# Kernel optimization log

Hardware: AMD Instinct MI355X
Metric: run time of the kernel (lower is better)

Reference implementation:

```python
import jax, jax.numpy as jnp
import numpy as np

SEQ, BATCH = 512, 256
INPUT_WIDTH, STATE_WIDTH = 64, 960
STREAM = INPUT_WIDTH + STATE_WIDTH  # 1024
OUTPUT_WIDTH = 128
P = 0.97  # identity_proportion


def _smooth_l1(pred, target):
    # torch.nn.SmoothL1Loss (beta=1, mean reduction)
    d = jnp.abs(pred - target)
    return jnp.mean(jnp.where(d < 1.0, 0.5 * d * d, d - 0.5))


def setup_inputs() -> dict:
    key = jax.random.key(0)
    k_in, k_st, k_w1, k_w2 = jax.random.split(key, 4)
    bound = float(np.sqrt(6.0 / (STREAM + STREAM)))  # xavier_uniform, gain=1
    return {
        "input": jax.random.normal(k_in, (SEQ, BATCH, INPUT_WIDTH), dtype=jnp.float32),
        "init_state": jax.random.normal(k_st, (BATCH, STREAM), dtype=jnp.float32),
        "aff_w": jnp.ones((STREAM,), dtype=jnp.float32),
        "aff_b": jnp.zeros((STREAM,), dtype=jnp.float32),
        "fc1_w": jax.random.uniform(k_w1, (STREAM, STREAM), minval=-bound, maxval=bound, dtype=jnp.float32),
        "fc1_b": jnp.zeros((STREAM,), dtype=jnp.float32),
        "fc2_w": jax.random.uniform(k_w2, (STREAM, STREAM), minval=-bound, maxval=bound, dtype=jnp.float32),
        "fc2_b": jnp.zeros((STREAM,), dtype=jnp.float32),
    }


def reference(input, init_state, aff_w, aff_b, fc1_w, fc1_b, fc2_w, fc2_b):
    iw = input.shape[-1]

    def res(s):
        # BatchNorm-style regularizer (torch.var -> unbiased, ddof=1)
        reg = _smooth_l1(s.mean(0), 0.0) + _smooth_l1(jnp.var(s, axis=0, ddof=1), 1.0)
        h = jnp.abs(s @ fc1_w.T + fc1_b)          # [B, STREAM]
        out = P * s + (1.0 - P) * (h @ fc2_w.T + fc2_b)
        return out, reg

    # step 0: overwrite + affine + res
    s = jnp.concatenate([input[0], init_state[:, iw:]], axis=-1)
    s = aff_w * s + aff_b
    s, reg0 = res(s)

    def body(s, elem):
        s = jnp.concatenate([elem, s[:, iw:]], axis=-1)  # Overwrite
        s, reg = res(s)
        return s, reg

    s, regs = jax.lax.scan(body, s, input[1:])
    out = s[:, -OUTPUT_WIDTH:]
    reg = jnp.concatenate([reg0[None], regs]).mean()
    return out, reg
```

## Files before the change

kernel.cpp:

```cpp
#include <hip/hip_runtime.h>
#include <stdint.h>
#include <stddef.h>

#define SEQ 512
#define BATCH 256
#define IW 64
#define STREAM 1024
#define OW 128

#define NGROUP 8
#define NSLICE 32
#define CW 32
#define RPG 32
#define NT 256

typedef __attribute__((ext_vector_type(4)))  float  f32x4;
typedef __attribute__((ext_vector_type(16))) float  f32x16;
typedef __attribute__((ext_vector_type(8)))  __bf16 bf16x8;
typedef __attribute__((ext_vector_type(8)))  short  short8;

__device__ __forceinline__ unsigned short f2bf(float x) {
  union { float f; uint32_t u; } v; v.f = x;
  return (unsigned short)((v.u + 0x7FFFu + ((v.u >> 16) & 1u)) >> 16);
}
__device__ __forceinline__ uint64_t pack4bf(f32x4 v) {
  return (uint64_t)f2bf(v[0]) | ((uint64_t)f2bf(v[1]) << 16)
       | ((uint64_t)f2bf(v[2]) << 32) | ((uint64_t)f2bf(v[3]) << 48);
}
__device__ __forceinline__ f32x4 ld_mall(const void* p) {
  f32x4 r;
  asm volatile("global_load_dwordx4 %0, %1, off sc0 sc1" : "=v"(r) : "v"(p) : "memory");
  return r;
}
__device__ __forceinline__ void st_mall(void* p, uint64_t v) {
  asm volatile("global_store_dwordx2 %0, %1, off sc0 sc1" :: "v"(p), "v"(v) : "memory");
}
#define WAIT_VM(N) do { asm volatile("s_waitcnt vmcnt(" #N ")" ::: "memory"); \
                        __builtin_amdgcn_sched_barrier(0); } while (0)

__device__ __forceinline__ int xoff(int rr, int k) {
  int c = k >> 3;
  return ((c >> 1) << 10) + ((c & 1) << 9) + (rr << 4) + ((k & 4) << 1);
}

#define WS_FLAGS   0
#define WS_SUMS    4096
#define WS_SUMS2   (4096 + 2097152)
#define WS_REGT    (4096 + 4194304)
#define WS_SBUF    (4096 + 4194304 + 4096)
#define WS_HBUF    (WS_SBUF + NGROUP*RPG*STREAM*2)
#define ZERO_BYTES (4096 + 4194304)

__global__ __launch_bounds__(NT, 1) void rnn_main(
    const float* __restrict__ input, const float* __restrict__ init_state,
    const float* __restrict__ aff_w, const float* __restrict__ aff_b,
    const float* __restrict__ fc1_w, const float* __restrict__ fc1_b,
    const float* __restrict__ fc2_w, const float* __restrict__ fc2_b,
    float* __restrict__ d_out, char* __restrict__ ws)
{
  __shared__ __align__(16) short W1s[NSLICE * STREAM];
  __shared__ __align__(16) short W2s[NSLICE * STREAM];
  __shared__ __align__(16) float partial[4 * RPG * CW];
  __shared__ __align__(16) float b1s[CW], b2s[CW];

  const int tid = threadIdx.x;
  const int g = blockIdx.x & 7;
  const int j = blockIdx.x >> 3;

  uint32_t* sflag = (uint32_t*)(ws + WS_FLAGS) + g * 32;
  uint32_t* hflag = (uint32_t*)(ws + WS_FLAGS + 1024) + g * 32;
  float* sumS  = (float*)(ws + WS_SUMS);
  float* sumS2 = (float*)(ws + WS_SUMS2);
  char* sbuf_c = ws + WS_SBUF + (size_t)g * (RPG * STREAM * 2);
  char* hbuf_c = ws + WS_HBUF + (size_t)g * (RPG * STREAM * 2);

  for (int idx = tid; idx < NSLICE * (STREAM / 8); idx += NT) {
    int n = idx >> 7;
    int kc = idx & 127;
    const float* p1 = fc1_w + (size_t)(j * CW + n) * STREAM + (kc << 3);
    const float* p2 = fc2_w + (size_t)(j * CW + n) * STREAM + (kc << 3);
    f32x4 a0 = *(const f32x4*)p1, a1 = *(const f32x4*)(p1 + 4);
    f32x4 c0 = *(const f32x4*)p2, c1 = *(const f32x4*)(p2 + 4);
    short8 w1v, w2v;
#pragma unroll
    for (int i = 0; i < 4; ++i) {
      w1v[i] = (short)f2bf(a0[i]); w1v[4 + i] = (short)f2bf(a1[i]);
      w2v[i] = (short)f2bf(c0[i]); w2v[4 + i] = (short)f2bf(c1[i]);
    }
    int boff = (n << 11) + ((kc << 4) ^ ((n & 7) << 4));
    *(short8*)((char*)W1s + boff) = w1v;
    *(short8*)((char*)W2s + boff) = w2v;
  }
  if (tid < CW) {
    b1s[tid] = fc1_b[j * CW + tid];
    b2s[tid] = fc2_b[j * CW + tid];
  }

  const int rr_ = tid >> 3;
  const int c4  = (tid & 7) << 2;
  const int gc  = j * CW + c4;
  f32x4 master = {0.f, 0.f, 0.f, 0.f};

  {
    f32x4 v;
    if (j >= 2) v = *(const f32x4*)(init_state + (size_t)(g * RPG + rr_) * STREAM + gc);
    else        v = *(const f32x4*)(input + (size_t)(g * RPG + rr_) * IW + gc);
    f32x4 w  = *(const f32x4*)(aff_w + gc);
    f32x4 bb = *(const f32x4*)(aff_b + gc);
    v = w * v + bb;
    if (j >= 2) master = v;
    st_mall(sbuf_c + xoff(rr_, gc), pack4bf(v));
    *(f32x4*)(partial + (rr_ << 5) + c4) = v;
  }
  WAIT_VM(0);
  __syncthreads();
  if (tid == 0)
    __hip_atomic_fetch_add(sflag, 1u, __ATOMIC_RELAXED, __HIP_MEMORY_SCOPE_AGENT);
  if (tid < CW) {
    float s1 = 0.f, s2 = 0.f;
#pragma unroll 4
    for (int r = 0; r < RPG; ++r) { float v = partial[(r << 5) + tid]; s1 += v; s2 += v * v; }
    atomicAdd(sumS  + j * CW + tid, s1);
    atomicAdd(sumS2 + j * CW + tid, s2);
  }

  const int ln  = tid & 63;
  const int wv  = tid >> 6;
  const int ar  = ln & 31;
  const int kof = (ln >> 5) << 3;
  const int klo = wv << 8;
  const int swzB = (ar & 7) << 4;
  const char* W1c = (const char*)W1s + (ar << 11);
  const char* W2c = (const char*)W2s + (ar << 11);
  const char* pa_s = sbuf_c + (wv << 14) + (ln << 4);
  const char* pa_h = hbuf_c + (wv << 14) + (ln << 4);

  for (int t = 0; t < SEQ; ++t) {
    if (tid == 0) {
      uint32_t tgt = 32u * (t + 1);
      while (__hip_atomic_load(sflag, __ATOMIC_RELAXED, __HIP_MEMORY_SCOPE_AGENT) < tgt)
        __builtin_amdgcn_s_sleep(1);
    }
    __syncthreads();

    {
      f32x4 a[16];
#pragma unroll
      for (int it = 0; it < 16; ++it) a[it] = ld_mall(pa_s + (it << 10));
      bf16x8 bf[16];
#pragma unroll
      for (int it = 0; it < 16; ++it)
        bf[it] = *(const bf16x8*)(W1c + (((klo + (it << 4) + kof) << 1) ^ swzB));
      f32x16 acc0 = {}, acc1 = {};
      WAIT_VM(8);
#pragma unroll
      for (int it = 0; it < 8; it += 2) {
        acc0 = __builtin_amdgcn_mfma_f32_32x32x16_bf16(__builtin_bit_cast(bf16x8, a[it]),     bf[it],     acc0, 0, 0, 0);
        acc1 = __builtin_amdgcn_mfma_f32_32x32x16_bf16(__builtin_bit_cast(bf16x8, a[it + 1]), bf[it + 1], acc1, 0, 0, 0);
      }
      WAIT_VM(0);
#pragma unroll
      for (int it = 8; it < 16; it += 2) {
        acc0 = __builtin_amdgcn_mfma_f32_32x32x16_bf16(__builtin_bit_cast(bf16x8, a[it]),     bf[it],     acc0, 0, 0, 0);
        acc1 = __builtin_amdgcn_mfma_f32_32x32x16_bf16(__builtin_bit_cast(bf16x8, a[it + 1]), bf[it + 1], acc1, 0, 0, 0);
      }
      acc0 += acc1;
      float* pw = partial + (wv << 10);
#pragma unroll
      for (int i = 0; i < 16; ++i) {
        int r = (i & 3) + ((i >> 2) << 3) + ((ln >> 5) << 2);
        pw[(r << 5) + (ln & 31)] = acc0[i];
      }
    }
    __syncthreads();
    {
      f32x4 sum = *(const f32x4*)(partial + (rr_ << 5) + c4);
      sum += *(const f32x4*)(partial + 1024 + (rr_ << 5) + c4);
      sum += *(const f32x4*)(partial + 2048 + (rr_ << 5) + c4);
      sum += *(const f32x4*)(partial + 3072 + (rr_ << 5) + c4);
      f32x4 vb = *(const f32x4*)(b1s + c4);
      f32x4 hv;
#pragma unroll
      for (int i = 0; i < 4; ++i) hv[i] = fabsf(sum[i] + vb[i]);
      st_mall(hbuf_c + xoff(rr_, gc), pack4bf(hv));
    }
    WAIT_VM(0);
    __syncthreads();
    if (tid == 0)
      __hip_atomic_fetch_add(hflag, 1u, __ATOMIC_RELAXED, __HIP_MEMORY_SCOPE_AGENT);

    if (tid == 0) {
      uint32_t tgt = 32u * (t + 1);
      while (__hip_atomic_load(hflag, __ATOMIC_RELAXED, __HIP_MEMORY_SCOPE_AGENT) < tgt)
        __builtin_amdgcn_s_sleep(1);
    }
    __syncthreads();

    f32x4 nxt = {0.f, 0.f, 0.f, 0.f};
    if (j >= 2) {
      f32x4 a[16];
#pragma unroll
      for (int it = 0; it < 16; ++it) a[it] = ld_mall(pa_h + (it << 10));
      bf16x8 bf[16];
#pragma unroll
      for (int it = 0; it < 16; ++it)
        bf[it] = *(const bf16x8*)(W2c + (((klo + (it << 4) + kof) << 1) ^ swzB));
      f32x16 acc0 = {}, acc1 = {};
      WAIT_VM(8);
#pragma unroll
      for (int it = 0; it < 8; it += 2) {
        acc0 = __builtin_amdgcn_mfma_f32_32x32x16_bf16(__builtin_bit_cast(bf16x8, a[it]),     bf[it],     acc0, 0, 0, 0);
        acc1 = __builtin_amdgcn_mfma_f32_32x32x16_bf16(__builtin_bit_cast(bf16x8, a[it + 1]), bf[it + 1], acc1, 0, 0, 0);
      }
      WAIT_VM(0);
#pragma unroll
      for (int it = 8; it < 16; it += 2) {
        acc0 = __builtin_amdgcn_mfma_f32_32x32x16_bf16(__builtin_bit_cast(bf16x8, a[it]),     bf[it],     acc0, 0, 0, 0);
        acc1 = __builtin_amdgcn_mfma_f32_32x32x16_bf16(__builtin_bit_cast(bf16x8, a[it + 1]), bf[it + 1], acc1, 0, 0, 0);
      }
      acc0 += acc1;
      float* pw = partial + (wv << 10);
#pragma unroll
      for (int i = 0; i < 16; ++i) {
        int r = (i & 3) + ((i >> 2) << 3) + ((ln >> 5) << 2);
        pw[(r << 5) + (ln & 31)] = acc0[i];
      }
      __syncthreads();
      f32x4 sum = *(const f32x4*)(partial + (rr_ << 5) + c4);
      sum += *(const f32x4*)(partial + 1024 + (rr_ << 5) + c4);
      sum += *(const f32x4*)(partial + 2048 + (rr_ << 5) + c4);
      sum += *(const f32x4*)(partial + 3072 + (rr_ << 5) + c4);
      f32x4 vb = *(const f32x4*)(b2s + c4);
#pragma unroll
      for (int i = 0; i < 4; ++i)
        master[i] = 0.97f * master[i] + 0.03f * (sum[i] + vb[i]);
      if (t < SEQ - 1)
        st_mall(sbuf_c + xoff(rr_, gc), pack4bf(master));
    } else {
      if (t < SEQ - 1) {
        nxt = *(const f32x4*)(input + ((size_t)(t + 1) * BATCH + g * RPG + rr_) * IW + gc);
        st_mall(sbuf_c + xoff(rr_, gc), pack4bf(nxt));
      }
    }

    __syncthreads();
    if (t < SEQ - 1)
      *(f32x4*)(partial + (rr_ << 5) + c4) = (j >= 2) ? master : nxt;
    WAIT_VM(0);
    __syncthreads();
    if (tid == 0)
      __hip_atomic_fetch_add(sflag, 1u, __ATOMIC_RELAXED, __HIP_MEMORY_SCOPE_AGENT);
    if (t < SEQ - 1 && tid < CW) {
      float s1 = 0.f, s2 = 0.f;
#pragma unroll 4
      for (int r = 0; r < RPG; ++r) { float v = partial[(r << 5) + tid]; s1 += v; s2 += v * v; }
      atomicAdd(sumS  + (size_t)(t + 1) * STREAM + j * CW + tid, s1);
      atomicAdd(sumS2 + (size_t)(t + 1) * STREAM + j * CW + tid, s2);
    }
  }

  if (j >= 28) {
    float* dst = d_out + (size_t)(g * RPG + rr_) * OW + (j - 28) * CW + c4;
    *(f32x4*)dst = master;
  }
}

__global__ void reg_reduce1(const float* __restrict__ sumS, const float* __restrict__ sumS2,
                            float* __restrict__ regt) {
  int t = blockIdx.x;
  float acc = 0.f;
  for (int c = threadIdx.x; c < STREAM; c += 256) {
    float s1 = sumS[t * STREAM + c];
    float s2 = sumS2[t * STREAM + c];
    float m = s1 * (1.0f / 256.0f);
    float var = (s2 - 256.0f * m * m) * (1.0f / 255.0f);
    float d1 = fabsf(m);
    acc += (d1 < 1.f) ? 0.5f * d1 * d1 : d1 - 0.5f;
    float d2 = fabsf(var - 1.f);
    acc += (d2 < 1.f) ? 0.5f * d2 * d2 : d2 - 0.5f;
  }
#pragma unroll
  for (int off = 32; off > 0; off >>= 1) acc += __shfl_down(acc, off, 64);
  __shared__ float red[4];
  if ((threadIdx.x & 63) == 0) red[threadIdx.x >> 6] = acc;
  __syncthreads();
  if (threadIdx.x == 0)
    regt[t] = (red[0] + red[1] + red[2] + red[3]) * (1.0f / 1024.0f);
}

__global__ void reg_reduce2(const float* __restrict__ regt, float* __restrict__ out_reg) {
  float acc = regt[threadIdx.x] + regt[threadIdx.x + 256];
#pragma unroll
  for (int off = 32; off > 0; off >>= 1) acc += __shfl_down(acc, off, 64);
  __shared__ float red[4];
  if ((threadIdx.x & 63) == 0) red[threadIdx.x >> 6] = acc;
  __syncthreads();
  if (threadIdx.x == 0)
    out_reg[0] = (red[0] + red[1] + red[2] + red[3]) * (1.0f / 512.0f);
}

extern "C" void kernel_launch(void* const* d_in, const int* in_sizes, int n_in,
                              void* d_out, int out_size, void* d_ws, size_t ws_size,
                              hipStream_t stream) {
  (void)in_sizes; (void)n_in; (void)out_size; (void)ws_size;
  const float* input      = (const float*)d_in[0];
  const float* init_state = (const float*)d_in[1];
  const float* aff_w      = (const float*)d_in[2];
  const float* aff_b      = (const float*)d_in[3];
  const float* fc1_w      = (const float*)d_in[4];
  const float* fc1_b      = (const float*)d_in[5];
  const float* fc2_w      = (const float*)d_in[6];
  const float* fc2_b      = (const float*)d_in[7];
  float* out = (float*)d_out;
  char* ws = (char*)d_ws;

  hipMemsetAsync(ws, 0, ZERO_BYTES, stream);

  void* args[] = { &input, &init_state, &aff_w, &aff_b, &fc1_w, &fc1_b, &fc2_w, &fc2_b, &out, &ws };
  hipError_t err = hipLaunchCooperativeKernel((void*)rnn_main, dim3(NGROUP * NSLICE), dim3(NT),
                                              args, 0, stream);
  if (err != hipSuccess) {
    hipLaunchKernelGGL(rnn_main, dim3(NGROUP * NSLICE), dim3(NT), 0, stream,
                       input, init_state, aff_w, aff_b, fc1_w, fc1_b, fc2_w, fc2_b, out, ws);
  }

  float* sumS  = (float*)(ws + WS_SUMS);
  float* sumS2 = (float*)(ws + WS_SUMS2);
  float* regt  = (float*)(ws + WS_REGT);
  hipLaunchKernelGGL(reg_reduce1, dim3(SEQ), dim3(256), 0, stream, sumS, sumS2, regt);
  hipLaunchKernelGGL(reg_reduce2, dim3(1), dim3(256), 0, stream, regt, out + 32768);
}
```

Measured before the change: 2.875 ms.

## Replace atomic counter barrier with per-block flag slots and per-wave waits

Swaps the shared atomic-counter barrier for one flag slot per producer block. Each block stores its step number with a plain system-coherent store. Each wave polls only the 8 slots for the K-range it consumes, so waves can start their MFMA work without a block-wide __syncthreads after the spin. This is meant to cut atomic contention and barrier latency on the per-step critical path. The cost is more polling traffic, plus an extra __syncthreads in the input-copy branch.

```diff
diff --git a/kernel.cpp b/kernel.cpp
--- a/kernel.cpp
+++ b/kernel.cpp
@@ -35,8 +35,23 @@
 __device__ __forceinline__ void st_mall(void* p, uint64_t v) {
   asm volatile("global_store_dwordx2 %0, %1, off sc0 sc1" :: "v"(p), "v"(v) : "memory");
 }
+__device__ __forceinline__ void st_mall32(void* p, uint32_t v) {
+  asm volatile("global_store_dword %0, %1, off sc0 sc1" :: "v"(p), "v"(v) : "memory");
+}
 #define WAIT_VM(N) do { asm volatile("s_waitcnt vmcnt(" #N ")" ::: "memory"); \
                         __builtin_amdgcn_sched_barrier(0); } while (0)
+
+__device__ __forceinline__ void wait8(const uint32_t* slots, uint32_t tgt, int l8) {
+  const uint32_t* p = slots + l8;
+  for (;;) {
+    uint32_t v;
+    asm volatile("global_load_dword %0, %1, off sc0 sc1" : "=v"(v) : "v"(p) : "memory");
+    asm volatile("s_waitcnt vmcnt(0)" ::: "memory");
+    if (__all((int)(v >= tgt))) break;
+    __builtin_amdgcn_s_sleep(1);
+  }
+  __builtin_amdgcn_sched_barrier(0);
+}
 
 __device__ __forceinline__ int xoff(int rr, int k) {
   int c = k >> 3;
@@ -67,8 +82,8 @@
   const int g = blockIdx.x & 7;
   const int j = blockIdx.x >> 3;
 
-  uint32_t* sflag = (uint32_t*)(ws + WS_FLAGS) + g * 32;
-  uint32_t* hflag = (uint32_t*)(ws + WS_FLAGS + 1024) + g * 32;
+  uint32_t* sslot = (uint32_t*)(ws + WS_FLAGS) + g * 64;
+  uint32_t* hslot = (uint32_t*)(ws + WS_FLAGS + 2048) + g * 64;
   float* sumS  = (float*)(ws + WS_SUMS);
   float* sumS2 = (float*)(ws + WS_SUMS2);
   char* sbuf_c = ws + WS_SBUF + (size_t)g * (RPG * STREAM * 2);
@@ -114,8 +129,7 @@
   }
   WAIT_VM(0);
   __syncthreads();
-  if (tid == 0)
-    __hip_atomic_fetch_add(sflag, 1u, __ATOMIC_RELAXED, __HIP_MEMORY_SCOPE_AGENT);
+  if (tid == 0) st_mall32(sslot + j, 1u);
   if (tid < CW) {
     float s1 = 0.f, s2 = 0.f;
 #pragma unroll 4
@@ -126,6 +140,7 @@
 
   const int ln  = tid & 63;
   const int wv  = tid >> 6;
+  const int l8  = ln & 7;
   const int ar  = ln & 31;
   const int kof = (ln >> 5) << 3;
   const int klo = wv << 8;
@@ -134,14 +149,11 @@
   const char* W2c = (const char*)W2s + (ar << 11);
   const char* pa_s = sbuf_c + (wv << 14) + (ln << 4);
   const char* pa_h = hbuf_c + (wv << 14) + (ln << 4);
+  const uint32_t* sw8 = sslot + 8 * wv;
+  const uint32_t* hw8 = hslot + 8 * wv;
 
   for (int t = 0; t < SEQ; ++t) {
-    if (tid == 0) {
-      uint32_t tgt = 32u * (t + 1);
-      while (__hip_atomic_load(sflag, __ATOMIC_RELAXED, __HIP_MEMORY_SCOPE_AGENT) < tgt)
-        __builtin_amdgcn_s_sleep(1);
-    }
-    __syncthreads();
+    wait8(sw8, (uint32_t)(t + 1), l8);
 
     {
       f32x4 a[16];
@@ -186,15 +198,9 @@
     }
     WAIT_VM(0);
     __syncthreads();
-    if (tid == 0)
-      __hip_atomic_fetch_add(hflag, 1u, __ATOMIC_RELAXED, __HIP_MEMORY_SCOPE_AGENT);
-
-    if (tid == 0) {
-      uint32_t tgt = 32u * (t + 1);
-      while (__hip_atomic_load(hflag, __ATOMIC_RELAXED, __HIP_MEMORY_SCOPE_AGENT) < tgt)
-        __builtin_amdgcn_s_sleep(1);
-    }
-    __syncthreads();
+    if (tid == 0) st_mall32(hslot + j, (uint32_t)(t + 1));
+
+    wait8(hw8, (uint32_t)(t + 1), l8);
 
     f32x4 nxt = {0.f, 0.f, 0.f, 0.f};
     if (j >= 2) {
@@ -237,10 +243,11 @@
       if (t < SEQ - 1)
         st_mall(sbuf_c + xoff(rr_, gc), pack4bf(master));
     } else {
-      if (t < SEQ - 1) {
+      if (t < SEQ - 1)
         nxt = *(const f32x4*)(input + ((size_t)(t + 1) * BATCH + g * RPG + rr_) * IW + gc);
+      __syncthreads();
+      if (t < SEQ - 1)
         st_mall(sbuf_c + xoff(rr_, gc), pack4bf(nxt));
-      }
     }
 
     __syncthreads();
@@ -248,8 +255,7 @@
       *(f32x4*)(partial + (rr_ << 5) + c4) = (j >= 2) ? master : nxt;
     WAIT_VM(0);
     __syncthreads();
-    if (tid == 0)
-      __hip_atomic_fetch_add(sflag, 1u, __ATOMIC_RELAXED, __HIP_MEMORY_SCOPE_AGENT);
+    if (tid == 0) st_mall32(sslot + j, (uint32_t)(t + 2));
     if (t < SEQ - 1 && tid < CW) {
       float s1 = 0.f, s2 = 0.f;
 #pragma unroll 4
```

After: 3.880 ms. 35.0% more time.
